# Kernel optimization log

Hardware: AMD Instinct MI355X
Metric: run time of the kernel (lower is better)

## Reference

```python
import jax, jax.numpy as jnp
import numpy as np

B, H, SQ, SK, D, INT, F = 1, 32, 2048, 2048, 128, 128, 32
THOLD = 0.5


def _mlp(x, W1, b1, W2, b2, W3, b3):
    # x: [b,h,s,d]; W*: [h,out,in] (torch Linear layout), y = x @ W^T + b, per head
    h = jax.nn.silu(jnp.einsum('bhsd,hid->bhsi', x, W1) + b1[None, :, None, :])
    h = jax.nn.silu(jnp.einsum('bhsi,hji->bhsj', h, W2) + b2[None, :, None, :])
    return jnp.einsum('bhsj,hfj->bhsf', h, W3) + b3[None, :, None, :]


def setup_inputs() -> dict:
    key = jax.random.key(0)
    ks = jax.random.split(key, 16)
    sc = 0.05  # small init so tanh stays in its linear-ish range
    inp = {
        'K': jax.random.normal(ks[0], (B, H, SK, D), jnp.float32),
        'Q': jax.random.normal(ks[1], (B, H, SQ, D), jnp.float32),
        'Wk1': jax.random.normal(ks[2], (H, INT, D), jnp.float32) * sc,
        'bk1': jax.random.normal(ks[3], (H, INT), jnp.float32) * sc,
        'Wk2': jax.random.normal(ks[4], (H, INT, INT), jnp.float32) * sc,
        'bk2': jax.random.normal(ks[5], (H, INT), jnp.float32) * sc,
        'Wk3': jax.random.normal(ks[6], (H, F, INT), jnp.float32) * sc,
        'bk3': jax.random.normal(ks[7], (H, F), jnp.float32) * sc,
        'Wq1': jax.random.normal(ks[8], (H, INT, D), jnp.float32) * sc,
        'bq1': jax.random.normal(ks[9], (H, INT), jnp.float32) * sc,
        'Wq2': jax.random.normal(ks[10], (H, INT, INT), jnp.float32) * sc,
        'bq2': jax.random.normal(ks[11], (H, INT), jnp.float32) * sc,
        'Wq3': jax.random.normal(ks[12], (H, F, INT), jnp.float32) * sc,
        'bq3': jax.random.normal(ks[13], (H, F), jnp.float32) * sc,
    }
    return inp


def reference(K, Q, Wk1, bk1, Wk2, bk2, Wk3, bk3, Wq1, bq1, Wq2, bq2, Wq3, bq3):
    # soft (hard=False) path of USA.forward
    Kl = jnp.tanh(_mlp(K, Wk1, bk1, Wk2, bk2, Wk3, bk3))  # [b,h,sk,F]
    Ql = jnp.tanh(_mlp(Q, Wq1, bq1, Wq2, bq2, Wq3, bq3))  # [b,h,sq,F]
    scores = jnp.einsum('bhtf,bhsf->bhts', Ql, Kl)        # [b,h,sq,sk]
    sq, sk = Q.shape[2], K.shape[2]
    causal = jnp.tril(jnp.ones((sq, sk), dtype=bool), k=sk - sq)
    mask_val = jnp.asarray(jnp.finfo(scores.dtype).min, scores.dtype)
    scores = jnp.where(causal[None, None], scores, mask_val)
    return jax.nn.sigmoid(scores - THOLD)
```

## Files before the change

### kernel.cpp

```cpp
#include <hip/hip_runtime.h>

#define NH  32
#define SEQ 2048
#define DIM 128
#define FD  32

typedef short          short8 __attribute__((ext_vector_type(8)));
typedef float          f32x4  __attribute__((ext_vector_type(4)));
typedef unsigned short u16x8  __attribute__((ext_vector_type(8)));

static __device__ __forceinline__ unsigned short f2bf(float f) {
    unsigned int u = __builtin_bit_cast(unsigned int, f);
    u += 0x7fffu + ((u >> 16) & 1u);
    return (unsigned short)(u >> 16);
}
static __device__ __forceinline__ float fexp(float x) {
    return __builtin_amdgcn_exp2f(x * 1.44269504088896f);
}
static __device__ __forceinline__ float sigm(float x) {
    return __builtin_amdgcn_rcpf(1.0f + fexp(-x));
}
static __device__ __forceinline__ float silu_f(float x) { return x * sigm(x); }
static __device__ __forceinline__ float tanh_f(float x) {
    return 1.0f - 2.0f * __builtin_amdgcn_rcpf(fexp(2.0f * x) + 1.0f);
}

#define WPH 36864
#define WPS (32 * WPH)

__global__ __launch_bounds__(256) void prep_weights(
    const float* __restrict__ Wk1, const float* __restrict__ Wk2,
    const float* __restrict__ Wk3, const float* __restrict__ Wq1,
    const float* __restrict__ Wq2, const float* __restrict__ Wq3,
    unsigned short* __restrict__ wimg) {
    int c = blockIdx.x * 256 + threadIdx.x;
    int s = (c >= 147456) ? 1 : 0;
    c -= s * 147456;
    const float* src;
    int dst;
    int sB = s * WPS;
    if (c < 65536) {
        int h = c >> 11, idx = c & 2047;
        int r = idx >> 4, jb = (idx & 15) * 8;
        src = (s ? Wq1 : Wk1) + h * 16384 + r * 128 + jb;
        dst = sB + h * WPH + r * 128 + (jb ^ ((r & 7) << 3));
    } else if (c < 131072) {
        int cc = c - 65536;
        int h = cc >> 11, idx = cc & 2047;
        int r = idx >> 4, jb = (idx & 15) * 8;
        src = (s ? Wq2 : Wk2) + h * 16384 + r * 128 + jb;
        dst = sB + h * WPH + 16384 + r * 128 + (jb ^ ((r & 7) << 3));
    } else {
        int cc = c - 131072;
        int h = cc >> 9, idx = cc & 511;
        int r = idx >> 4, jb = (idx & 15) * 8;
        src = (s ? Wq3 : Wk3) + h * 4096 + r * 128 + jb;
        dst = sB + h * WPH + 32768 + r * 128 + (jb ^ ((r & 7) << 3));
    }
    f32x4 u0 = *(const f32x4*)src;
    f32x4 u1 = *(const f32x4*)(src + 4);
    u16x8 p;
    p[0] = f2bf(u0[0]); p[1] = f2bf(u0[1]); p[2] = f2bf(u0[2]); p[3] = f2bf(u0[3]);
    p[4] = f2bf(u1[0]); p[5] = f2bf(u1[1]); p[6] = f2bf(u1[2]); p[7] = f2bf(u1[3]);
    *(u16x8*)(&wimg[dst]) = p;
}

template <int OT, int ACT>
static __device__ __forceinline__ void compute_layer(
    const short8 a[4], const unsigned short* W,
    const float* __restrict__ bias, unsigned short* dst, int lane, int wid) {
    int r0 = lane & 15, q = lane >> 4, kb = q * 8;
#pragma unroll
    for (int ot = 0; ot < OT; ++ot) {
        int wrow = ot * 16 + r0;
        int sw   = (wrow & 7) << 3;
        short8 b[4];
#pragma unroll
        for (int ks = 0; ks < 4; ++ks)
            b[ks] = *(const short8*)(&W[wrow * 128 + ((ks * 32 + kb) ^ sw)]);
        f32x4 acc = {0.f, 0.f, 0.f, 0.f};
#pragma unroll
        for (int ks = 0; ks < 4; ++ks)
            acc = __builtin_amdgcn_mfma_f32_16x16x32_bf16(a[ks], b[ks], acc, 0, 0, 0);
        float bv = bias[wrow];
#pragma unroll
        for (int r = 0; r < 4; ++r) {
            float y = acc[r] + bv;
            float v = (ACT == 0) ? silu_f(y) : tanh_f(y);
            int orow = wid * 16 + q * 4 + r;
            int ocol = ot * 16 + r0;
            dst[orow * 128 + (ocol ^ ((orow & 7) << 3))] = f2bf(v);
        }
    }
}

static __device__ __forceinline__ void compute_layer3_reg(
    const short8 a[4], const short8 w3f[2][4],
    const float* __restrict__ bias, unsigned short* dst, int lane, int wid) {
    int r0 = lane & 15, q = lane >> 4;
#pragma unroll
    for (int ot = 0; ot < 2; ++ot) {
        f32x4 acc = {0.f, 0.f, 0.f, 0.f};
#pragma unroll
        for (int ks = 0; ks < 4; ++ks)
            acc = __builtin_amdgcn_mfma_f32_16x16x32_bf16(a[ks], w3f[ot][ks], acc, 0, 0, 0);
        float bv = bias[ot * 16 + r0];
#pragma unroll
        for (int r = 0; r < 4; ++r) {
            float v = tanh_f(acc[r] + bv);
            dst[(wid * 16 + q * 4 + r) * FD + ot * 16 + r0] = f2bf(v);
        }
    }
}

__global__ __launch_bounds__(256) void mlp_kernel(
    const float* __restrict__ K,  const float* __restrict__ Q,
    const float* __restrict__ bk1, const float* __restrict__ bk2,
    const float* __restrict__ bk3, const float* __restrict__ bq1,
    const float* __restrict__ bq2, const float* __restrict__ bq3,
    const unsigned short* __restrict__ wimg,
    unsigned short* __restrict__ Kl, unsigned short* __restrict__ Ql) {
    __shared__ unsigned short wb[128 * 128];
    __shared__ unsigned short act[64 * 128];
    __shared__ unsigned short outb[64 * FD];
    int raw = blockIdx.x;
    int bid = (raw & 7) * 256 + (raw >> 3);
    int tb  = bid & 31;
    int h   = (bid >> 5) & 31;
    int s   = bid >> 10;

    const float* X  = s ? Q : K;
    const unsigned short* Wb = wimg + s * WPS + h * WPH;
    const float* B1 = (s ? bq1 : bk1) + h * 128;
    const float* B2 = (s ? bq2 : bk2) + h * 128;
    const float* B3 = (s ? bq3 : bk3) + h * FD;
    unsigned short* gout = (s ? Ql : Kl) + ((size_t)h * SEQ + (size_t)tb * 64) * FD;

    int tid = threadIdx.x, lane = tid & 63, wid = tid >> 6;
    int r0 = lane & 15, kb = (lane >> 4) * 8;

    short8 w3f[2][4];
    {
        const unsigned short* W3g = Wb + 32768;
        int sw = (r0 & 7) << 3;
#pragma unroll
        for (int ot = 0; ot < 2; ++ot)
#pragma unroll
            for (int ks = 0; ks < 4; ++ks)
                w3f[ot][ks] = *(const short8*)(&W3g[(ot * 16 + r0) * 128 + ((ks * 32 + kb) ^ sw)]);
    }

    const u16x8* wsrc = (const u16x8*)Wb;
#pragma unroll
    for (int i = 0; i < 8; ++i)
        *(u16x8*)(&wb[(i * 256 + tid) * 8]) = wsrc[i * 256 + tid];

    short8 a[4];
    const float* xs = X + ((size_t)h * SEQ + (size_t)tb * 64) * DIM;
    int row = wid * 16 + r0;
#pragma unroll
    for (int ks = 0; ks < 4; ++ks) {
        const float* p = xs + row * 128 + ks * 32 + kb;
        f32x4 u0 = *(const f32x4*)p;
        f32x4 u1 = *(const f32x4*)(p + 4);
        short8 t;
        t[0] = f2bf(u0[0]); t[1] = f2bf(u0[1]); t[2] = f2bf(u0[2]); t[3] = f2bf(u0[3]);
        t[4] = f2bf(u1[0]); t[5] = f2bf(u1[1]); t[6] = f2bf(u1[2]); t[7] = f2bf(u1[3]);
        a[ks] = t;
    }
    __syncthreads();
    compute_layer<8, 0>(a, wb, B1, act, lane, wid);
    __syncthreads();
#pragma unroll
    for (int i = 0; i < 8; ++i)
        *(u16x8*)(&wb[(i * 256 + tid) * 8]) = wsrc[2048 + i * 256 + tid];
    __syncthreads();
    {
        int sw = (row & 7) << 3;
#pragma unroll
        for (int ks = 0; ks < 4; ++ks)
            a[ks] = *(const short8*)(&act[row * 128 + ((ks * 32 + kb) ^ sw)]);
    }
    compute_layer<8, 0>(a, wb, B2, act, lane, wid);
    {
        int sw = (row & 7) << 3;
#pragma unroll
        for (int ks = 0; ks < 4; ++ks)
            a[ks] = *(const short8*)(&act[row * 128 + ((ks * 32 + kb) ^ sw)]);
    }
    compute_layer3_reg(a, w3f, B3, outb, lane, wid);
    __syncthreads();
    *(u16x8*)(gout + tid * 8) = *(const u16x8*)(&outb[tid * 8]);
}

__global__ __launch_bounds__(256) void score_kernel(
    const unsigned short* __restrict__ Ql, const unsigned short* __restrict__ Kl,
    float* __restrict__ out) {
    int raw = blockIdx.x;
    int bid = (raw & 7) * 512 + (raw >> 3);
    int h   = bid >> 7;
    int i   = (bid >> 2) & 31;
    int j   = bid & 3;
    int tq0 = i * 64, tk0 = j * 512;
    int tid = threadIdx.x;
    float* ob = out + (size_t)h * SEQ * SEQ;

    if (tk0 > tq0 + 63) {
        f32x4 z = {0.f, 0.f, 0.f, 0.f};
#pragma unroll
        for (int it = 0; it < 8; ++it) {
            int row = tq0 + it * 8 + (tid >> 5);
            float* dst = ob + (size_t)row * SEQ + tk0 + (tid & 31) * 4;
#pragma unroll
            for (int rep = 0; rep < 4; ++rep)
                *(f32x4*)(dst + rep * 128) = z;
        }
        return;
    }
    bool diag = (tk0 + 511 > tq0);
    __shared__ float sb[16 * 516];
    int lane = tid & 63;
    int w    = tid >> 6;
    int r0   = lane & 15;
    int q    = lane >> 4;
    int kb   = q * 8;

    short8 aq[4], bk[8];
#pragma unroll
    for (int p = 0; p < 4; ++p)
        aq[p] = *(const short8*)(Ql + ((size_t)h * SEQ + tq0 + p * 16 + r0) * FD + kb);
#pragma unroll
    for (int ct = 0; ct < 8; ++ct)
        bk[ct] = *(const short8*)(Kl + ((size_t)h * SEQ + tk0 + w * 128 + ct * 16 + r0) * FD + kb);

#pragma unroll
    for (int p = 0; p < 4; ++p) {
#pragma unroll
        for (int ct = 0; ct < 8; ++ct) {
            f32x4 acc = {0.f, 0.f, 0.f, 0.f};
            acc = __builtin_amdgcn_mfma_f32_16x16x32_bf16(aq[p], bk[ct], acc, 0, 0, 0);
            int colw = w * 128 + ct * 16 + r0;
#pragma unroll
            for (int r = 0; r < 4; ++r) {
                int lr = q * 4 + r;
                float o = sigm(acc[r] - 0.5f);
                if (diag && (tk0 + colw) > (tq0 + p * 16 + lr)) o = 0.0f;
                sb[lr * 516 + colw] = o;
            }
        }
        asm volatile("s_waitcnt lgkmcnt(0)" ::: "memory");
        __builtin_amdgcn_s_barrier();
#pragma unroll
        for (int rr = 0; rr < 4; ++rr) {
            int srow = w * 4 + rr;
            const float* src = &sb[srow * 516];
            float* dst = ob + (size_t)(tq0 + p * 16 + srow) * SEQ + tk0;
#pragma unroll
            for (int rep = 0; rep < 2; ++rep) {
                f32x4 v = *(const f32x4*)(src + lane * 4 + rep * 256);
                *(f32x4*)(dst + lane * 4 + rep * 256) = v;
            }
        }
        __builtin_amdgcn_s_barrier();
    }
}

extern "C" void kernel_launch(void* const* d_in, const int* in_sizes, int n_in,
                              void* d_out, int out_size, void* d_ws, size_t ws_size,
                              hipStream_t stream) {
    const float* K   = (const float*)d_in[0];
    const float* Q   = (const float*)d_in[1];
    const float* Wk1 = (const float*)d_in[2];
    const float* bk1 = (const float*)d_in[3];
    const float* Wk2 = (const float*)d_in[4];
    const float* bk2 = (const float*)d_in[5];
    const float* Wk3 = (const float*)d_in[6];
    const float* bk3 = (const float*)d_in[7];
    const float* Wq1 = (const float*)d_in[8];
    const float* bq1 = (const float*)d_in[9];
    const float* Wq2 = (const float*)d_in[10];
    const float* bq2 = (const float*)d_in[11];
    const float* Wq3 = (const float*)d_in[12];
    const float* bq3 = (const float*)d_in[13];

    unsigned short* Kl   = (unsigned short*)d_ws;
    unsigned short* Ql   = Kl + (size_t)NH * SEQ * FD;
    unsigned short* wimg = Ql + (size_t)NH * SEQ * FD;

    prep_weights<<<dim3(1152), dim3(256), 0, stream>>>(
        Wk1, Wk2, Wk3, Wq1, Wq2, Wq3, wimg);

    mlp_kernel<<<dim3(2 * NH * (SEQ / 64)), dim3(256), 0, stream>>>(
        K, Q, bk1, bk2, bk3, bq1, bq2, bq3, wimg, Kl, Ql);

    score_kernel<<<dim3(NH * 32 * 4), dim3(256), 0, stream>>>(
        Ql, Kl, (float*)d_out);
}
```

Measured before the change: 141.0 us.

## Stream MLP weights in half-tiles with register prefetch and fold log2e into Kl

The MLP kernel now stages weights in 64-row halves through a smaller LDS buffer. The next half is prefetched into registers while the current half is computed, and launch bounds request higher occupancy. The Kl output is pre-scaled by log2e so the score kernel's sigmoid uses exp2 directly, saving a multiply. This adds more barriers and changes bf16 rounding of Kl slightly. The score kernel is likely bound by output stores, which limits how much the change can help.

```diff
diff --git a/kernel.cpp b/kernel.cpp
--- a/kernel.cpp
+++ b/kernel.cpp
@@ -65,38 +65,40 @@
     *(u16x8*)(&wimg[dst]) = p;
 }
 
-template <int OT, int ACT>
-static __device__ __forceinline__ void compute_layer(
-    const short8 a[4], const unsigned short* W,
-    const float* __restrict__ bias, unsigned short* dst, int lane, int wid) {
+template <int ACT>
+static __device__ __forceinline__ void compute_half(
+    const short8 a[4], const unsigned short* wb,
+    const float* __restrict__ bias, int obase,
+    unsigned short* act, int lane, int wid) {
     int r0 = lane & 15, q = lane >> 4, kb = q * 8;
 #pragma unroll
-    for (int ot = 0; ot < OT; ++ot) {
-        int wrow = ot * 16 + r0;
-        int sw   = (wrow & 7) << 3;
+    for (int ot = 0; ot < 4; ++ot) {
+        int lr = ot * 16 + r0;
+        int sw = (lr & 7) << 3;
         short8 b[4];
 #pragma unroll
         for (int ks = 0; ks < 4; ++ks)
-            b[ks] = *(const short8*)(&W[wrow * 128 + ((ks * 32 + kb) ^ sw)]);
+            b[ks] = *(const short8*)(&wb[lr * 128 + ((ks * 32 + kb) ^ sw)]);
         f32x4 acc = {0.f, 0.f, 0.f, 0.f};
 #pragma unroll
         for (int ks = 0; ks < 4; ++ks)
             acc = __builtin_amdgcn_mfma_f32_16x16x32_bf16(a[ks], b[ks], acc, 0, 0, 0);
-        float bv = bias[wrow];
+        float bv = bias[obase + lr];
 #pragma unroll
         for (int r = 0; r < 4; ++r) {
             float y = acc[r] + bv;
             float v = (ACT == 0) ? silu_f(y) : tanh_f(y);
             int orow = wid * 16 + q * 4 + r;
-            int ocol = ot * 16 + r0;
-            dst[orow * 128 + (ocol ^ ((orow & 7) << 3))] = f2bf(v);
+            int ocol = obase + ot * 16 + r0;
+            act[orow * 128 + (ocol ^ ((orow & 7) << 3))] = f2bf(v);
         }
     }
 }
 
 static __device__ __forceinline__ void compute_layer3_reg(
     const short8 a[4], const short8 w3f[2][4],
-    const float* __restrict__ bias, unsigned short* dst, int lane, int wid) {
+    const float* __restrict__ bias, float oscale,
+    unsigned short* dst, int lane, int wid) {
     int r0 = lane & 15, q = lane >> 4;
 #pragma unroll
     for (int ot = 0; ot < 2; ++ot) {
@@ -107,20 +109,20 @@
         float bv = bias[ot * 16 + r0];
 #pragma unroll
         for (int r = 0; r < 4; ++r) {
-            float v = tanh_f(acc[r] + bv);
+            float v = tanh_f(acc[r] + bv) * oscale;
             dst[(wid * 16 + q * 4 + r) * FD + ot * 16 + r0] = f2bf(v);
         }
     }
 }
 
-__global__ __launch_bounds__(256) void mlp_kernel(
+__global__ __launch_bounds__(256, 4) void mlp_kernel(
     const float* __restrict__ K,  const float* __restrict__ Q,
     const float* __restrict__ bk1, const float* __restrict__ bk2,
     const float* __restrict__ bk3, const float* __restrict__ bq1,
     const float* __restrict__ bq2, const float* __restrict__ bq3,
     const unsigned short* __restrict__ wimg,
     unsigned short* __restrict__ Kl, unsigned short* __restrict__ Ql) {
-    __shared__ unsigned short wb[128 * 128];
+    __shared__ unsigned short wb[64 * 128];
     __shared__ unsigned short act[64 * 128];
     __shared__ unsigned short outb[64 * FD];
     int raw = blockIdx.x;
@@ -139,6 +141,12 @@
     int tid = threadIdx.x, lane = tid & 63, wid = tid >> 6;
     int r0 = lane & 15, kb = (lane >> 4) * 8;
 
+    const u16x8* wsrc = (const u16x8*)Wb;
+    u16x8 pf[4];
+
+#pragma unroll
+    for (int i = 0; i < 4; ++i) pf[i] = wsrc[i * 256 + tid];
+
     short8 w3f[2][4];
     {
         const unsigned short* W3g = Wb + 32768;
@@ -149,11 +157,6 @@
             for (int ks = 0; ks < 4; ++ks)
                 w3f[ot][ks] = *(const short8*)(&W3g[(ot * 16 + r0) * 128 + ((ks * 32 + kb) ^ sw)]);
     }
-
-    const u16x8* wsrc = (const u16x8*)Wb;
-#pragma unroll
-    for (int i = 0; i < 8; ++i)
-        *(u16x8*)(&wb[(i * 256 + tid) * 8]) = wsrc[i * 256 + tid];
 
     short8 a[4];
     const float* xs = X + ((size_t)h * SEQ + (size_t)tb * 64) * DIM;
@@ -168,27 +171,45 @@
         t[4] = f2bf(u1[0]); t[5] = f2bf(u1[1]); t[6] = f2bf(u1[2]); t[7] = f2bf(u1[3]);
         a[ks] = t;
     }
-    __syncthreads();
-    compute_layer<8, 0>(a, wb, B1, act, lane, wid);
-    __syncthreads();
-#pragma unroll
-    for (int i = 0; i < 8; ++i)
-        *(u16x8*)(&wb[(i * 256 + tid) * 8]) = wsrc[2048 + i * 256 + tid];
-    __syncthreads();
+
+#pragma unroll
+    for (int i = 0; i < 4; ++i) *(u16x8*)(&wb[(i * 256 + tid) * 8]) = pf[i];
+    __syncthreads();
+#pragma unroll
+    for (int i = 0; i < 4; ++i) pf[i] = wsrc[1024 + i * 256 + tid];
+    compute_half<0>(a, wb, B1, 0, act, lane, wid);
+    __syncthreads();
+#pragma unroll
+    for (int i = 0; i < 4; ++i) *(u16x8*)(&wb[(i * 256 + tid) * 8]) = pf[i];
+    __syncthreads();
+#pragma unroll
+    for (int i = 0; i < 4; ++i) pf[i] = wsrc[2048 + i * 256 + tid];
+    compute_half<0>(a, wb, B1, 64, act, lane, wid);
+    __syncthreads();
+#pragma unroll
+    for (int i = 0; i < 4; ++i) *(u16x8*)(&wb[(i * 256 + tid) * 8]) = pf[i];
+    __syncthreads();
+#pragma unroll
+    for (int i = 0; i < 4; ++i) pf[i] = wsrc[3072 + i * 256 + tid];
     {
         int sw = (row & 7) << 3;
 #pragma unroll
         for (int ks = 0; ks < 4; ++ks)
             a[ks] = *(const short8*)(&act[row * 128 + ((ks * 32 + kb) ^ sw)]);
     }
-    compute_layer<8, 0>(a, wb, B2, act, lane, wid);
+    compute_half<0>(a, wb, B2, 0, act, lane, wid);
+    __syncthreads();
+#pragma unroll
+    for (int i = 0; i < 4; ++i) *(u16x8*)(&wb[(i * 256 + tid) * 8]) = pf[i];
+    __syncthreads();
+    compute_half<0>(a, wb, B2, 64, act, lane, wid);
     {
         int sw = (row & 7) << 3;
 #pragma unroll
         for (int ks = 0; ks < 4; ++ks)
             a[ks] = *(const short8*)(&act[row * 128 + ((ks * 32 + kb) ^ sw)]);
     }
-    compute_layer3_reg(a, w3f, B3, outb, lane, wid);
+    compute_layer3_reg(a, w3f, B3, s ? 1.0f : 1.44269504f, outb, lane, wid);
     __syncthreads();
     *(u16x8*)(gout + tid * 8) = *(const u16x8*)(&outb[tid * 8]);
 }
@@ -243,7 +264,8 @@
 #pragma unroll
             for (int r = 0; r < 4; ++r) {
                 int lr = q * 4 + r;
-                float o = sigm(acc[r] - 0.5f);
+                float e = __builtin_amdgcn_exp2f(0.72134752f - acc[r]);
+                float o = __builtin_amdgcn_rcpf(1.0f + e);
                 if (diag && (tk0 + colw) > (tq0 + p * 16 + lr)) o = 0.0f;
                 sb[lr * 516 + colw] = o;
             }
```

After: 147.1 us. +4.3%, slower.
